# Kernel optimization log

Measured on AMD Instinct MI355X. Metric: run time of the kernel, lower is better.

## Reference

```python
import jax, jax.numpy as jnp
import numpy as np

N_CODEBOOKS = 4
CODEBOOK_DIM = 12
CODEBOOK_SIZE = 4096  # 2 ** CODEBOOK_DIM
BATCH = 8192
COMMIT_W = 0.1
CODEBOOK_W = 0.1
ENTROPY_W = 1.0
EPS = 1e-9


def _base_codes():
    # all 2^D sign patterns in {-1, +1}^D, shape [K, D]
    idx = jnp.arange(CODEBOOK_SIZE)
    bits = (idx[:, None] >> jnp.arange(CODEBOOK_DIM)[None, :]) & 1
    return bits.astype(jnp.float32) * 2.0 - 1.0


def setup_inputs() -> dict:
    key = jax.random.key(0)
    x = jax.random.normal(key, (BATCH, CODEBOOK_DIM), dtype=jnp.float32)
    return {"x": x}


def _lfq(residual, scale, codes):
    # sign-based quantization at this codebook's scale
    q = jnp.where(residual > 0, scale, -scale)  # [B, D]
    commit = jnp.mean((residual - jax.lax.stop_gradient(q)) ** 2)
    codebook = jnp.mean((jax.lax.stop_gradient(residual) - q) ** 2)
    # entropy aux loss over all 2^D codewords (logits ~ -||x-c||^2 up to row consts)
    logits = 2.0 * jnp.einsum("bd,kd->bk", residual, codes * scale)  # [B, K]
    logp = jax.nn.log_softmax(logits, axis=-1)
    p = jnp.exp(logp)
    per_sample_entropy = -jnp.mean(jnp.sum(p * logp, axis=-1))
    avg_p = jnp.mean(p, axis=0)
    codebook_entropy = -jnp.sum(avg_p * jnp.log(avg_p + EPS))
    entropy_loss = per_sample_entropy - codebook_entropy
    # straight-through estimator
    q_st = residual + jax.lax.stop_gradient(q - residual)
    loss = COMMIT_W * commit + CODEBOOK_W * codebook + ENTROPY_W * entropy_loss
    return q_st, loss, commit, codebook, entropy_loss


def _forward(x):
    codes = _base_codes()
    scales = 2.0 ** (-jnp.arange(N_CODEBOOKS, dtype=jnp.float32))

    def step(carry, scale):
        xh, residual = carry
        q, l, c, cb, e = _lfq(residual, scale, codes)
        return (xh + q, residual - q), jnp.stack([l, c, cb, e])

    (xh, _), losses = jax.lax.scan(step, (jnp.zeros_like(x), x), scales)
    tot = jnp.sum(losses, axis=0)  # summed over codebooks
    return xh, tot[0], tot[1], tot[2], tot[3]


def reference(x):
    # returns (x_hat, total_loss, commit_loss, codebook_loss, entropy_loss)
    return _forward(x)
```

## Files before the change

### kernel.cpp

```cpp
#include <hip/hip_runtime.h>
#include <math.h>

#define BATCH 8192
#define NCB 4
#define NBINS 4096
#define HBINS (NCB * NBINS)
#define NBLK 256
#define SPB 32

#define PART_OFF 0
#define CPART_OFF (NBLK * HBINS)
#define HPART_OFF (CPART_OFF + NBLK)
#define CEPART_OFF (HPART_OFF + NBLK)
#define CNT_OFF (CEPART_OFF + NBLK)

__global__ __launch_bounds__(256)
void lfq_fused_kernel(const float* __restrict__ x, float* __restrict__ out,
                      float* __restrict__ ws) {
    __shared__ float P[32 * 68];
    __shared__ __align__(16) float T[64 * 128];
    __shared__ float CS[4], HS[4];

    const int t = threadIdx.x, w = t >> 6, lane = t & 63;
    const int blk = blockIdx.x;
    const int b0 = blk * SPB;

    if (blk == 0 && t == 0) *(unsigned*)(ws + CNT_OFF) = 0u;

    float csum = 0.f, hsum = 0.f;
    if (t < 192) {
        const int s = t & 31, dp = t >> 5;
        float2 xv = *(const float2*)(x + (b0 + s) * 12 + 2 * dp);
        float r0 = xv.x, r1 = xv.y;
        float xh0 = 0.f, xh1 = 0.f;
        const float scales[4] = {1.f, 0.5f, 0.25f, 0.125f};
#pragma unroll
        for (int cb = 0; cb < 4; ++cb) {
            const float sc = scales[cb];
            float q0 = (r0 > 0.f) ? sc : -sc;
            float q1 = (r1 > 0.f) ? sc : -sc;
            float d0 = r0 - q0, d1 = r1 - q1;
            csum += d0 * d0 + d1 * d1;
            float a0 = 2.f * sc * r0, a1 = 2.f * sc * r1;
            float m0 = fabsf(a0), m1 = fabsf(a1);
            float u0 = __expf(-2.f * m0), u1 = __expf(-2.f * m1);
            float i0 = __builtin_amdgcn_rcpf(1.f + u0);
            float i1 = __builtin_amdgcn_rcpf(1.f + u1);
            hsum += m0 + __logf(1.f + u0) - m0 * (1.f - u0) * i0;
            hsum += m1 + __logf(1.f + u1) - m1 * (1.f - u1) * i1;
            float pp0 = (a0 >= 0.f) ? i0 : u0 * i0;
            float pp1 = (a1 >= 0.f) ? i1 : u1 * i1;
            *(float2*)(&P[s * 68 + cb * 16 + 2 * dp]) = make_float2(pp0, pp1);
            xh0 += q0;
            xh1 += q1;
            r0 = d0;
            r1 = d1;
        }
        *(float2*)(out + (b0 + s) * 12 + 2 * dp) = make_float2(xh0, xh1);
    }
#pragma unroll
    for (int off = 32; off; off >>= 1) {
        csum += __shfl_down(csum, off);
        hsum += __shfl_down(hsum, off);
    }
    if (lane == 0) {
        CS[w] = csum;
        HS[w] = hsum;
    }
    __syncthreads();
    if (t == 0) {
        ws[CPART_OFF + blk] = CS[0] + CS[1] + CS[2] + CS[3];
        ws[HPART_OFF + blk] = HS[0] + HS[1] + HS[2] + HS[3];
    }

    float acc[4][16];
#pragma unroll
    for (int cb = 0; cb < 4; ++cb)
#pragma unroll
        for (int i = 0; i < 16; ++i) acc[cb][i] = 0.f;

    const int lg = lane & 15, lh = lane >> 4;

    for (int round = 0; round < 2; ++round) {
        __syncthreads();
        const int sbase = round * 16;
        for (int i = 0; i < 16; ++i) {
            const float* pp = &P[(sbase + i) * 68 + w * 16];
            float4 pA = *(const float4*)pp;
            float4 pB = *(const float4*)(pp + 4);
            float4 pC = *(const float4*)(pp + 8);
            float L = (lane & 1) ? pA.x : 1.f - pA.x;
            L *= (lane & 2) ? pA.y : 1.f - pA.y;
            L *= (lane & 4) ? pA.z : 1.f - pA.z;
            L *= (lane & 8) ? pA.w : 1.f - pA.w;
            L *= (lane & 16) ? pB.x : 1.f - pB.x;
            L *= (lane & 32) ? pB.y : 1.f - pB.y;
            float H = (lane & 1) ? pB.z : 1.f - pB.z;
            H *= (lane & 2) ? pB.w : 1.f - pB.w;
            H *= (lane & 4) ? pC.x : 1.f - pC.x;
            H *= (lane & 8) ? pC.y : 1.f - pC.y;
            H *= (lane & 16) ? pC.z : 1.f - pC.z;
            H *= (lane & 32) ? pC.w : 1.f - pC.w;
            float* Trow = &T[(i * 4 + w) * 128];
            Trow[lane] = L;
            Trow[64 + lane] = H;
        }
        __syncthreads();
#pragma unroll 2
        for (int s = 0; s < 16; ++s) {
#pragma unroll
            for (int cb = 0; cb < 4; ++cb) {
                const float* Ts = &T[(s * 4 + cb) * 128];
                float4 L4 = *(const float4*)(Ts + 4 * lg);
                float4 H4 = *(const float4*)(Ts + 64 + 16 * w + 4 * lh);
                acc[cb][0] += H4.x * L4.x;
                acc[cb][1] += H4.x * L4.y;
                acc[cb][2] += H4.x * L4.z;
                acc[cb][3] += H4.x * L4.w;
                acc[cb][4] += H4.y * L4.x;
                acc[cb][5] += H4.y * L4.y;
                acc[cb][6] += H4.y * L4.z;
                acc[cb][7] += H4.y * L4.w;
                acc[cb][8] += H4.z * L4.x;
                acc[cb][9] += H4.z * L4.y;
                acc[cb][10] += H4.z * L4.z;
                acc[cb][11] += H4.z * L4.w;
                acc[cb][12] += H4.w * L4.x;
                acc[cb][13] += H4.w * L4.y;
                acc[cb][14] += H4.w * L4.z;
                acc[cb][15] += H4.w * L4.w;
            }
        }
    }
    float* mp = ws + PART_OFF + (size_t)blk * HBINS;
#pragma unroll
    for (int cb = 0; cb < 4; ++cb)
#pragma unroll
        for (int hh = 0; hh < 4; ++hh) {
            int hi = 16 * w + 4 * lh + hh;
            *(float4*)(mp + cb * NBINS + hi * 64 + 4 * lg) =
                make_float4(acc[cb][hh * 4 + 0], acc[cb][hh * 4 + 1],
                            acc[cb][hh * 4 + 2], acc[cb][hh * 4 + 3]);
        }
}

__global__ __launch_bounds__(256)
void lfq_reduce_kernel(const float* __restrict__ part, float* __restrict__ ws,
                       float* __restrict__ out) {
    const int t = threadIdx.x, w = t >> 6, lane = t & 63;
    const int bin = blockIdx.x * 64 + lane;
    const float* p = part + (size_t)(w * 64) * HBINS + bin;
    float s0 = 0.f, s1 = 0.f, s2 = 0.f, s3 = 0.f;
#pragma unroll 4
    for (int j = 0; j < 64; j += 4) {
        s0 += p[(size_t)(j + 0) * HBINS];
        s1 += p[(size_t)(j + 1) * HBINS];
        s2 += p[(size_t)(j + 2) * HBINS];
        s3 += p[(size_t)(j + 3) * HBINS];
    }
    __shared__ float S[4][64];
    S[w][lane] = s0 + s1 + s2 + s3;
    __syncthreads();
    if (w == 0) {
        float tot = S[0][lane] + S[1][lane] + S[2][lane] + S[3][lane];
        float avgp = tot * (1.f / 8192.f);
        float ce = avgp * __logf(avgp + 1e-9f);
#pragma unroll
        for (int off = 32; off; off >>= 1) ce += __shfl_down(ce, off);
        if (lane == 0) ws[CEPART_OFF + blockIdx.x] = ce;
    }
    __threadfence();
    __shared__ int lastFlag;
    if (t == 0) {
        unsigned old = atomicAdd((unsigned*)(ws + CNT_OFF), 1u);
        lastFlag = (old == NBLK - 1);
    }
    __syncthreads();
    if (lastFlag) {
        __threadfence();
        float ce2 = ws[CEPART_OFF + t];
        float cs = ws[CPART_OFF + t];
        float hs = ws[HPART_OFF + t];
#pragma unroll
        for (int off = 32; off; off >>= 1) {
            ce2 += __shfl_down(ce2, off);
            cs += __shfl_down(cs, off);
            hs += __shfl_down(hs, off);
        }
        __shared__ float R[3][4];
        if (lane == 0) {
            R[0][w] = ce2;
            R[1][w] = cs;
            R[2][w] = hs;
        }
        __syncthreads();
        if (t == 0) {
            float cesum = R[0][0] + R[0][1] + R[0][2] + R[0][3];
            float commit = (R[1][0] + R[1][1] + R[1][2] + R[1][3]) *
                           (1.f / (8192.f * 12.f));
            float pse =
                (R[2][0] + R[2][1] + R[2][2] + R[2][3]) * (1.f / 8192.f);
            float codebook_entropy = -cesum;
            float entropy_loss = pse - codebook_entropy;
            float loss = 0.2f * commit + entropy_loss;
            out[BATCH * 12 + 0] = loss;
            out[BATCH * 12 + 1] = commit;
            out[BATCH * 12 + 2] = commit;
            out[BATCH * 12 + 3] = entropy_loss;
        }
    }
}

extern "C" void kernel_launch(void* const* d_in, const int* in_sizes, int n_in,
                              void* d_out, int out_size, void* d_ws,
                              size_t ws_size, hipStream_t stream) {
    const float* x = (const float*)d_in[0];
    float* out = (float*)d_out;
    float* ws = (float*)d_ws;

    hipLaunchKernelGGL(lfq_fused_kernel, dim3(NBLK), dim3(256), 0, stream, x,
                       out, ws);
    hipLaunchKernelGGL(lfq_reduce_kernel, dim3(NBLK), dim3(256), 0, stream,
                       ws + PART_OFF, ws, out);
}
```

Measured before the change: 46.64 us.

## Assign each wave its own codebook outer product to drop block barriers

Each wave now accumulates the full 64x64 outer-product histogram for the one codebook it builds itself, using an 8x8 register tile per lane, instead of splitting each codebook's bins across all four waves. Because each wave only reads T rows it wrote, the two __syncthreads per round are removed. The per-lane accumulator count stays at 64 and the number of LDS loads per FMA improves. A risk is that register pressure from the 8x8 tile could lower occupancy.

```diff
diff --git a/kernel.cpp b/kernel.cpp
--- a/kernel.cpp
+++ b/kernel.cpp
@@ -22,8 +22,7 @@
     __shared__ float CS[4], HS[4];
 
     const int t = threadIdx.x, w = t >> 6, lane = t & 63;
-    const int blk = blockIdx.x;
-    const int b0 = blk * SPB;
+    const int blk = blockIdx.x, b0 = blk * SPB;
 
     if (blk == 0 && t == 0) *(unsigned*)(ws + CNT_OFF) = 0u;
 
@@ -73,16 +72,14 @@
         ws[HPART_OFF + blk] = HS[0] + HS[1] + HS[2] + HS[3];
     }
 
-    float acc[4][16];
-#pragma unroll
-    for (int cb = 0; cb < 4; ++cb)
-#pragma unroll
-        for (int i = 0; i < 16; ++i) acc[cb][i] = 0.f;
-
-    const int lg = lane & 15, lh = lane >> 4;
+    const int lo0 = 8 * (lane & 7), hi0 = 8 * (lane >> 3);
+    float acc[8][8];
+#pragma unroll
+    for (int i = 0; i < 8; ++i)
+#pragma unroll
+        for (int j = 0; j < 8; ++j) acc[i][j] = 0.f;
 
     for (int round = 0; round < 2; ++round) {
-        __syncthreads();
         const int sbase = round * 16;
         for (int i = 0; i < 16; ++i) {
             const float* pp = &P[(sbase + i) * 68 + w * 16];
@@ -105,43 +102,30 @@
             Trow[lane] = L;
             Trow[64 + lane] = H;
         }
-        __syncthreads();
 #pragma unroll 2
-        for (int s = 0; s < 16; ++s) {
-#pragma unroll
-            for (int cb = 0; cb < 4; ++cb) {
-                const float* Ts = &T[(s * 4 + cb) * 128];
-                float4 L4 = *(const float4*)(Ts + 4 * lg);
-                float4 H4 = *(const float4*)(Ts + 64 + 16 * w + 4 * lh);
-                acc[cb][0] += H4.x * L4.x;
-                acc[cb][1] += H4.x * L4.y;
-                acc[cb][2] += H4.x * L4.z;
-                acc[cb][3] += H4.x * L4.w;
-                acc[cb][4] += H4.y * L4.x;
-                acc[cb][5] += H4.y * L4.y;
-                acc[cb][6] += H4.y * L4.z;
-                acc[cb][7] += H4.y * L4.w;
-                acc[cb][8] += H4.z * L4.x;
-                acc[cb][9] += H4.z * L4.y;
-                acc[cb][10] += H4.z * L4.z;
-                acc[cb][11] += H4.z * L4.w;
-                acc[cb][12] += H4.w * L4.x;
-                acc[cb][13] += H4.w * L4.y;
-                acc[cb][14] += H4.w * L4.z;
-                acc[cb][15] += H4.w * L4.w;
-            }
-        }
-    }
-    float* mp = ws + PART_OFF + (size_t)blk * HBINS;
-#pragma unroll
-    for (int cb = 0; cb < 4; ++cb)
-#pragma unroll
-        for (int hh = 0; hh < 4; ++hh) {
-            int hi = 16 * w + 4 * lh + hh;
-            *(float4*)(mp + cb * NBINS + hi * 64 + 4 * lg) =
-                make_float4(acc[cb][hh * 4 + 0], acc[cb][hh * 4 + 1],
-                            acc[cb][hh * 4 + 2], acc[cb][hh * 4 + 3]);
-        }
+        for (int i = 0; i < 16; ++i) {
+            const float* Ts = &T[(i * 4 + w) * 128];
+            float4 La = *(const float4*)(Ts + lo0);
+            float4 Lb = *(const float4*)(Ts + lo0 + 4);
+            float4 Ha = *(const float4*)(Ts + 64 + hi0);
+            float4 Hb = *(const float4*)(Ts + 64 + hi0 + 4);
+            float Lv[8] = {La.x, La.y, La.z, La.w, Lb.x, Lb.y, Lb.z, Lb.w};
+            float Hv[8] = {Ha.x, Ha.y, Ha.z, Ha.w, Hb.x, Hb.y, Hb.z, Hb.w};
+#pragma unroll
+            for (int ii = 0; ii < 8; ++ii)
+#pragma unroll
+                for (int jj = 0; jj < 8; ++jj)
+                    acc[ii][jj] += Hv[ii] * Lv[jj];
+        }
+    }
+    float* mp = ws + PART_OFF + (size_t)blk * HBINS + w * NBINS;
+#pragma unroll
+    for (int ii = 0; ii < 8; ++ii) {
+        *(float4*)(mp + (hi0 + ii) * 64 + lo0) =
+            make_float4(acc[ii][0], acc[ii][1], acc[ii][2], acc[ii][3]);
+        *(float4*)(mp + (hi0 + ii) * 64 + lo0 + 4) =
+            make_float4(acc[ii][4], acc[ii][5], acc[ii][6], acc[ii][7]);
+    }
 }
 
 __global__ __launch_bounds__(256)
```

After: 45.93 us. Within noise of the previous version (-1.5%).
